# Kernel optimization log

Measured on AMD Instinct MI355X. Metric: run time of the kernel, lower is better.

## Reference

```python
import jax, jax.numpy as jnp
import numpy as np

B, S, E, G, O, TOPK = 4, 2048, 1024, 8, 4096, 2


def setup_inputs() -> dict:
    key = jax.random.key(0)
    k1, k2, k3, k4 = jax.random.split(key, 4)
    return {
        "hidden_states": jax.random.normal(k1, (B, S, E), dtype=jnp.float32),
        "WG": jax.random.normal(k2, (E, G), dtype=jnp.float32) * (1.0 / np.sqrt(E)),
        "Wi": jax.random.normal(k3, (G, E, O), dtype=jnp.float32) * (1.0 / np.sqrt(E)),
        "down": jax.random.normal(k4, (O, E), dtype=jnp.float32) * (1.0 / np.sqrt(O)),
        "topk": TOPK,
    }


def reference(hidden_states, WG, Wi, down, topk):
    # gate logits: [b, s, g]
    gate = jnp.matmul(hidden_states, WG)
    # sparse path (smoe_fwd): topk mask zeroes non-selected gate LOGITS,
    # so non-selected experts get sigmoid(0) = 0.5 (faithful to source).
    _, idx = jax.lax.top_k(gate, topk)              # [b, s, topk]
    mask = jnp.max(jax.nn.one_hot(idx, gate.shape[-1], dtype=gate.dtype), axis=-2)  # [b, s, g]
    w = jax.nn.sigmoid(gate * mask)                  # [b, s, g]
    # weighted combination over all expert matrices: [b, s, o]
    y = jnp.einsum('bse,bsg,geo->bso', hidden_states, w, Wi)
    # squared ReLU
    h = jnp.square(jax.nn.relu(y))
    return jnp.matmul(h, down)                       # [b, s, e]
```

## Files before the change

### kernel.cpp

```cpp
#include <hip/hip_runtime.h>
#include <hip/hip_bf16.h>
#include <math.h>

typedef __bf16 bf16;
typedef __bf16 bf16x4 __attribute__((ext_vector_type(4)));
typedef __bf16 bf16x8 __attribute__((ext_vector_type(8)));
typedef float  floatx4 __attribute__((ext_vector_type(4)));

#define N_TOK 8192
#define E_DIM 1024
#define G_DIM 8
#define O_DIM 4096
#define EPI_LD 132

__device__ __forceinline__ void gload_lds16(const void* g, void* l) {
    __builtin_amdgcn_global_load_lds(
        (__attribute__((address_space(1))) void*)(g),
        (__attribute__((address_space(3))) void*)(l),
        16, 0, 0);
}

__global__ __launch_bounds__(256) void gate_compute(
    const float* __restrict__ X,
    const float* __restrict__ WG,
    int* __restrict__ sel,
    float* __restrict__ sval)
{
    __shared__ float lwgT[G_DIM * E_DIM];
    const int tid  = threadIdx.x;
    const int wave = tid >> 6;
    const int lane = tid & 63;

#pragma unroll
    for (int k = 0; k < 8; ++k) {
        const int i = k * 256 + tid;
        const float4 v = *(const float4*)(WG + i * 4);
        const int e  = i >> 1;
        const int g0 = (i & 1) * 4;
        lwgT[(g0 + 0) * E_DIM + e] = v.x;
        lwgT[(g0 + 1) * E_DIM + e] = v.y;
        lwgT[(g0 + 2) * E_DIM + e] = v.z;
        lwgT[(g0 + 3) * E_DIM + e] = v.w;
    }
    __syncthreads();

    const int t = blockIdx.x * 4 + wave;
    float acc[G_DIM];
#pragma unroll
    for (int g = 0; g < G_DIM; ++g) acc[g] = 0.f;

#pragma unroll
    for (int it = 0; it < 4; ++it) {
        const int e0 = it * 256 + lane * 4;
        const float4 xv = *(const float4*)(X + (long)t * E_DIM + e0);
#pragma unroll
        for (int g = 0; g < G_DIM; ++g) {
            const float4 wv = *(const float4*)(lwgT + g * E_DIM + e0);
            acc[g] += xv.x * wv.x + xv.y * wv.y + xv.z * wv.z + xv.w * wv.w;
        }
    }
#pragma unroll
    for (int g = 0; g < G_DIM; ++g) {
        float v = acc[g];
#pragma unroll
        for (int off = 32; off > 0; off >>= 1) v += __shfl_down(v, off, 64);
        acc[g] = v;
    }
    if (lane == 0) {
        int i1 = 0;
#pragma unroll
        for (int g = 1; g < G_DIM; ++g) if (acc[g] > acc[i1]) i1 = g;
        int i2 = (i1 == 0) ? 1 : 0;
#pragma unroll
        for (int g = 0; g < G_DIM; ++g)
            if (g != i1 && g != i2 && acc[g] > acc[i2]) i2 = g;
#pragma unroll
        for (int s = 0; s < 2; ++s) {
            const int g = s ? i2 : i1;
            sel[t * 2 + s]  = g;
            sval[t * 2 + s] = 1.f / (1.f + expf(-acc[g])) - 0.5f;
        }
    }
}

__global__ __launch_bounds__(1024) void route_kernel(
    const int* __restrict__ sel, const float* __restrict__ sval,
    int* __restrict__ cnt, int* __restrict__ off, int* __restrict__ offp,
    int* __restrict__ tok, float* __restrict__ scl, int* __restrict__ pos)
{
    __shared__ int hcnt[16][G_DIM];
    __shared__ int wbase[16][G_DIM];
    const int tid  = threadIdx.x;
    const int w    = tid >> 6;
    const int lane = tid & 63;
    const unsigned long long below = ((unsigned long long)1 << lane) - 1;

    int c0[G_DIM];
#pragma unroll
    for (int g = 0; g < G_DIM; ++g) c0[g] = 0;
    for (int c = 0; c < 16; ++c) {
        const int g = sel[w * 1024 + c * 64 + lane];
#pragma unroll
        for (int gg = 0; gg < G_DIM; ++gg)
            c0[gg] += __popcll(__ballot(g == gg));
    }
    if (lane == 0)
#pragma unroll
        for (int g = 0; g < G_DIM; ++g) hcnt[w][g] = c0[g];
    __syncthreads();

    if (tid == 0) {
        int tot[G_DIM];
#pragma unroll
        for (int g = 0; g < G_DIM; ++g) {
            int a = 0;
            for (int ww = 0; ww < 16; ++ww) { wbase[ww][g] = a; a += hcnt[ww][g]; }
            tot[g] = a; cnt[g] = a;
        }
        int a = 0, b = 0;
#pragma unroll
        for (int g = 0; g < G_DIM; ++g) {
            off[g]  = a; a += tot[g];
            offp[g] = b; b += (tot[g] + 127) & ~127;
        }
        offp[G_DIM] = b;
    }
    __syncthreads();

    int run[G_DIM];
#pragma unroll
    for (int g = 0; g < G_DIM; ++g) run[g] = 0;
    for (int c = 0; c < 16; ++c) {
        const int idx = w * 1024 + c * 64 + lane;
        const int g   = sel[idx];
        const float sv = sval[idx];
        int myrank = 0;
#pragma unroll
        for (int gg = 0; gg < G_DIM; ++gg) {
            const unsigned long long m = __ballot(g == gg);
            const int r = run[gg] + __popcll(m & below);
            if (g == gg) myrank = r;
            run[gg] += __popcll(m);
        }
        const int p = wbase[w][g] + myrank;
        tok[g * N_TOK + p] = idx >> 1;
        scl[g * N_TOK + p] = sv;
        pos[idx] = (g << 16) | p;
    }
}

__global__ __launch_bounds__(256) void convert_x(
    const float* __restrict__ X, bf16* __restrict__ Xb)
{
    const long i = ((long)blockIdx.x * 256 + threadIdx.x) * 4;
    const float4 v = *(const float4*)(X + i);
    bf16x4 o;
    o[0] = (bf16)v.x; o[1] = (bf16)v.y; o[2] = (bf16)v.z; o[3] = (bf16)v.w;
    *(bf16x4*)(Xb + i) = o;
}

__global__ __launch_bounds__(256) void transpose_conv(
    const float* __restrict__ S, bf16* __restrict__ D, int R, int C)
{
    __shared__ float tile[64][65];
    const int r0  = blockIdx.x * 64;
    const int c0  = blockIdx.y * 64;
    const int tid = threadIdx.x;
    const int tr  = tid >> 4;
    const int tc4 = (tid & 15) * 4;

#pragma unroll
    for (int p = 0; p < 4; ++p) {
        const int r = p * 16 + tr;
        const float4 v = *(const float4*)(S + (long)(r0 + r) * C + c0 + tc4);
        tile[r][tc4 + 0] = v.x;
        tile[r][tc4 + 1] = v.y;
        tile[r][tc4 + 2] = v.z;
        tile[r][tc4 + 3] = v.w;
    }
    __syncthreads();
#pragma unroll
    for (int p = 0; p < 4; ++p) {
        const int c = p * 16 + tr;
        bf16x4 o;
        o[0] = (bf16)tile[tc4 + 0][c];
        o[1] = (bf16)tile[tc4 + 1][c];
        o[2] = (bf16)tile[tc4 + 2][c];
        o[3] = (bf16)tile[tc4 + 3][c];
        *(bf16x4*)(D + (long)(c0 + c) * R + r0 + tc4) = o;
    }
}

__global__ __launch_bounds__(256) void wsum_kernel(
    const bf16* __restrict__ WiT, bf16* __restrict__ WsumT)
{
    const int o  = blockIdx.x;
    const int e4 = threadIdx.x * 4;
    float a0 = 0.f, a1 = 0.f, a2 = 0.f, a3 = 0.f;
#pragma unroll
    for (int g = 0; g < G_DIM; ++g) {
        const bf16x4 v = *(const bf16x4*)(WiT + (long)o * 8192 + g * E_DIM + e4);
        a0 += (float)v[0]; a1 += (float)v[1]; a2 += (float)v[2]; a3 += (float)v[3];
    }
    bf16x4 w;
    w[0] = (bf16)(0.5f * a0); w[1] = (bf16)(0.5f * a1);
    w[2] = (bf16)(0.5f * a2); w[3] = (bf16)(0.5f * a3);
    *(bf16x4*)(WsumT + (long)o * E_DIM + e4) = w;
}

__global__ __launch_bounds__(128) void gather_rows(
    const bf16* __restrict__ Xb, const int* __restrict__ cnt,
    const int* __restrict__ offp, const int* __restrict__ tok,
    bf16* __restrict__ Xs)
{
    const int slot = blockIdx.x;
    if (slot >= offp[G_DIM]) return;
    int g = 0;
    while (slot >= offp[g + 1]) ++g;
    const int p = slot - offp[g];
    bf16* dst = Xs + (long)slot * E_DIM + threadIdx.x * 8;
    if (p < cnt[g]) {
        const bf16* src = Xb + (long)tok[g * N_TOK + p] * E_DIM + threadIdx.x * 8;
        *(bf16x8*)dst = *(const bf16x8*)src;
    } else {
        bf16x8 z = {};
        *(bf16x8*)dst = z;
    }
}

__device__ __forceinline__ void gemm_core256(
    const bf16* __restrict__ Ap, long lda,
    const bf16* __restrict__ Bp, long ldb,
    int K, char* smem, floatx4 (&acc)[8][4])
{
    const int tid  = threadIdx.x;
    const int wave = tid >> 6;
    const int lane = tid & 63;
    const int wm   = wave >> 2;
    const int wn   = wave & 3;
    const int fr   = lane & 15;
    const int fq   = lane >> 4;

#pragma unroll
    for (int i = 0; i < 8; ++i)
#pragma unroll
        for (int j = 0; j < 4; ++j)
            acc[i][j] = (floatx4){0.f, 0.f, 0.f, 0.f};

    const int  srow = tid >> 2;
    const int  ksw  = (((tid & 3) ^ ((tid >> 3) & 3)) << 4);
    const char* sa  = (const char*)Ap + (long)srow * (lda * 2) + ksw;
    const char* sb  = (const char*)Bp + (long)srow * (ldb * 2) + ksw;
    const long aR   = lda * 256;
    const long bR   = ldb * 256;
    const int  ldsW = wave * 1024;

#define STAGE_H(sbase, src, rstr, kb) do {                                   \
        gload_lds16((src) + (kb),          smem + (sbase) + ldsW);           \
        gload_lds16((src) + (kb) + (rstr), smem + (sbase) + 8192 + ldsW);    \
    } while (0)

    const int asw = ((fq ^ ((fr >> 1) & 3)) << 4);
    const int aro = (wm * 128 + fr) * 64 + asw;
    const int bro = (wn * 64 + fr) * 64 + asw;

    const int nt = K >> 6;

    {
        const long k1 = (nt > 1) ? 128 : 0;
        STAGE_H(0,             sa, aR, 0);
        STAGE_H(32768,         sb, bR, 0);
        STAGE_H(16384,         sa, aR, 64);
        STAGE_H(49152,         sb, bR, 64);
        STAGE_H(65536 + 32768, sb, bR, k1);
        STAGE_H(65536 + 0,     sa, aR, k1);
    }
    asm volatile("s_waitcnt vmcnt(4)" ::: "memory");
    __builtin_amdgcn_s_barrier();

#define LD8(v, off) (v) = *(const bf16x8*)(smem + (off))
#define PHASE_MID()   __builtin_amdgcn_s_barrier()
#define PHASE_END()   __builtin_amdgcn_s_barrier()
#define PHASE_END_V() do {                                                   \
        asm volatile("s_waitcnt vmcnt(8)" ::: "memory");                     \
        __builtin_amdgcn_s_barrier();                                        \
    } while (0)

    bf16x8 af[4], bq[4];

    for (int t = 0; t < nt; ++t) {
        const int  bo  = (t & 1) << 16;
        const int  nbo = bo ^ 65536;
        const long k1  = (long)((t + 1 < nt) ? t + 1 : nt - 1) * 128;
        const long k2  = (long)((t + 2 < nt) ? t + 2 : nt - 1) * 128;

#pragma unroll
        for (int i = 0; i < 4; ++i) LD8(af[i], bo + aro + i * 1024);
#pragma unroll
        for (int j = 0; j < 4; ++j) LD8(bq[j], bo + 32768 + bro + j * 1024);
        STAGE_H(nbo + 49152, sb, bR, k1 + 64);
        PHASE_MID();
        __builtin_amdgcn_s_setprio(1);
#pragma unroll
        for (int i = 0; i < 4; ++i)
#pragma unroll
            for (int j = 0; j < 4; ++j)
                acc[i][j] = __builtin_amdgcn_mfma_f32_16x16x32_bf16(
                    af[i], bq[j], acc[i][j], 0, 0, 0);
        __builtin_amdgcn_s_setprio(0);
        PHASE_END();

#pragma unroll
        for (int i = 0; i < 4; ++i) LD8(af[i], bo + aro + 4096 + i * 1024);
        STAGE_H(nbo + 16384, sa, aR, k1 + 64);
        PHASE_MID();
        __builtin_amdgcn_s_setprio(1);
#pragma unroll
        for (int i = 0; i < 4; ++i)
#pragma unroll
            for (int j = 0; j < 4; ++j)
                acc[4 + i][j] = __builtin_amdgcn_mfma_f32_16x16x32_bf16(
                    af[i], bq[j], acc[4 + i][j], 0, 0, 0);
        __builtin_amdgcn_s_setprio(0);
        PHASE_END_V();

#pragma unroll
        for (int i = 0; i < 4; ++i) LD8(af[i], bo + 16384 + aro + i * 1024);
#pragma unroll
        for (int j = 0; j < 4; ++j) LD8(bq[j], bo + 49152 + bro + j * 1024);
        STAGE_H(bo + 32768, sb, bR, k2);
        PHASE_MID();
        __builtin_amdgcn_s_setprio(1);
#pragma unroll
        for (int i = 0; i < 4; ++i)
#pragma unroll
            for (int j = 0; j < 4; ++j)
                acc[i][j] = __builtin_amdgcn_mfma_f32_16x16x32_bf16(
                    af[i], bq[j], acc[i][j], 0, 0, 0);
        __builtin_amdgcn_s_setprio(0);
        PHASE_END();

#pragma unroll
        for (int i = 0; i < 4; ++i) LD8(af[i], bo + 16384 + aro + 4096 + i * 1024);
        STAGE_H(bo + 0, sa, aR, k2);
        PHASE_MID();
        __builtin_amdgcn_s_setprio(1);
#pragma unroll
        for (int i = 0; i < 4; ++i)
#pragma unroll
            for (int j = 0; j < 4; ++j)
                acc[4 + i][j] = __builtin_amdgcn_mfma_f32_16x16x32_bf16(
                    af[i], bq[j], acc[4 + i][j], 0, 0, 0);
        __builtin_amdgcn_s_setprio(0);
        PHASE_END_V();
    }

    asm volatile("s_waitcnt vmcnt(0)" ::: "memory");
    __builtin_amdgcn_s_barrier();
#undef STAGE_H
#undef LD8
#undef PHASE_MID
#undef PHASE_END
#undef PHASE_END_V
}

__global__ __launch_bounds__(512, 2) void gemm256_base(
    const bf16* __restrict__ A, const bf16* __restrict__ BT,
    bf16* __restrict__ C)
{
    __shared__ __align__(16) char smem[131072];
    const int u   = blockIdx.x;
    const int xcd = u & 7;
    const int s   = u >> 3;
    const int mt  = s & 31;
    const int ct  = xcd + 8 * (s >> 5);
    const int row0 = mt * 256, col0 = ct * 256;

    floatx4 acc[8][4];
    gemm_core256(A + (long)row0 * E_DIM, E_DIM,
                 BT + (long)col0 * E_DIM, E_DIM,
                 E_DIM, smem, acc);

    const int tid = threadIdx.x, wave = tid >> 6, lane = tid & 63;
    const int wm = wave >> 2, wn = wave & 3, fr = lane & 15, fq = lane >> 4;
    bf16* tile = (bf16*)smem;
#pragma unroll
    for (int i = 0; i < 8; ++i)
#pragma unroll
        for (int j = 0; j < 4; ++j)
#pragma unroll
            for (int r = 0; r < 4; ++r)
                tile[(wm * 128 + i * 16 + fq * 4 + r) * 256 + wn * 64 + j * 16 + fr] =
                    (bf16)(acc[i][j][r]);
    __syncthreads();
#pragma unroll
    for (int k = 0; k < 16; ++k) {
        const int rl = (tid >> 5) + k * 16;
        const int cc = (tid & 31) * 8;
        *(bf16x8*)(C + (long)(row0 + rl) * O_DIM + col0 + cc) =
            *(const bf16x8*)(tile + rl * 256 + cc);
    }
}

__global__ __launch_bounds__(512, 2) void gemm256_sparse(
    const bf16* __restrict__ Xs,
    const bf16* __restrict__ WiT,
    const int* __restrict__ cnt,
    const int* __restrict__ off,
    const int* __restrict__ offp,
    const float* __restrict__ scl,
    bf16* __restrict__ ysp)
{
    const int u   = blockIdx.x;
    const int xcd = u & 7;
    const int s   = u >> 3;
    const int mt  = s & 63;
    const int pc  = xcd + 8 * (s >> 6);
    const int g   = pc & 7;
    const int ct  = pc >> 3;

    const int cg     = cnt[g];
    const int base_p = offp[g];
    const int cgp    = offp[g + 1] - base_p;
    const int m0     = mt * 256;
    if (m0 >= cgp) return;

    __shared__ __align__(16) char smem[131072];
    const int col0 = ct * 256;

    floatx4 acc[8][4];
    gemm_core256(Xs + (long)(base_p + m0) * E_DIM, E_DIM,
                 WiT + (long)col0 * 8192 + g * E_DIM, 8192,
                 E_DIM, smem, acc);

    const int tid = threadIdx.x, wave = tid >> 6, lane = tid & 63;
    const int wm = wave >> 2, wn = wave & 3, fr = lane & 15, fq = lane >> 4;
    const float* sclg = scl + g * N_TOK;
    const int clmax = cg - 1;
    bf16* tile = (bf16*)smem;
#pragma unroll
    for (int i = 0; i < 8; ++i)
#pragma unroll
        for (int r = 0; r < 4; ++r) {
            const int rl = wm * 128 + i * 16 + fq * 4 + r;
            const int gm = m0 + rl;
            const float sv = sclg[gm > clmax ? clmax : gm];
#pragma unroll
            for (int j = 0; j < 4; ++j)
                tile[rl * 256 + wn * 64 + j * 16 + fr] = (bf16)(sv * acc[i][j][r]);
        }
    __syncthreads();
    const long ob = off[g] + m0;
#pragma unroll
    for (int k = 0; k < 16; ++k) {
        const int rl = (tid >> 5) + k * 16;
        if (m0 + rl < cg) {
            const int cc = (tid & 31) * 8;
            *(bf16x8*)(ysp + (ob + rl) * O_DIM + col0 + cc) =
                *(const bf16x8*)(tile + rl * 256 + cc);
        }
    }
}

template <typename OUT, bool VEC>
__global__ __launch_bounds__(256, 4) void gemm_mt(
    const bf16* __restrict__ A, int lda,
    const bf16* __restrict__ BT, int ldb,
    OUT* __restrict__ C, int ldc, int K)
{
    __shared__ char smem[VEC ? (128 * EPI_LD * 2) : 16384];
    bf16* As = (bf16*)smem;
    bf16* Bs = (bf16*)(smem + 8192);

    const int u   = blockIdx.x;
    const int xcd = u & 7;
    const int s   = u >> 3;
    const int mt  = s & 63;
    const int col = xcd + 8 * (s >> 6);

    const int tid  = threadIdx.x;
    const int wave = tid >> 6;
    const int lane = tid & 63;
    const int row0 = mt * 128;
    const int col0 = col * 128;

    const int sr = lane >> 2;
    const int sc = (lane & 3) * 8;
    const bf16* agp0 = A  + (long)(row0 + 16 * wave       + sr) * lda + sc;
    const bf16* agp1 = A  + (long)(row0 + 16 * (wave + 4) + sr) * lda + sc;
    const bf16* bgp0 = BT + (long)(col0 + 16 * wave       + sr) * ldb + sc;
    const bf16* bgp1 = BT + (long)(col0 + 16 * (wave + 4) + sr) * ldb + sc;
    bf16* asl0 = As + (long)wave * 512;
    bf16* asl1 = As + (long)(wave + 4) * 512;
    bf16* bsl0 = Bs + (long)wave * 512;
    bf16* bsl1 = Bs + (long)(wave + 4) * 512;

    const int mi_base = (wave >> 1) * 64;
    const int ni_base = (wave & 1) * 64;
    const int fr = lane & 15;
    const int fq = lane >> 4;

    floatx4 acc[4][4] = {};

    for (int k0 = 0; k0 < K; k0 += 32) {
        __syncthreads();
        gload_lds16(agp0 + k0, (void*)asl0);
        gload_lds16(agp1 + k0, (void*)asl1);
        gload_lds16(bgp0 + k0, (void*)bsl0);
        gload_lds16(bgp1 + k0, (void*)bsl1);
        __syncthreads();

        bf16x8 af[4], bfr[4];
#pragma unroll
        for (int i = 0; i < 4; ++i) {
            af[i]  = *(const bf16x8*)(As + (mi_base + i * 16 + fr) * 32 + fq * 8);
            bfr[i] = *(const bf16x8*)(Bs + (ni_base + i * 16 + fr) * 32 + fq * 8);
        }
#pragma unroll
        for (int i = 0; i < 4; ++i)
#pragma unroll
            for (int j = 0; j < 4; ++j)
                acc[i][j] = __builtin_amdgcn_mfma_f32_16x16x32_bf16(
                    af[i], bfr[j], acc[i][j], 0, 0, 0);
    }

    if (VEC) {
        __syncthreads();
        bf16* tile = (bf16*)smem;
#pragma unroll
        for (int i = 0; i < 4; ++i)
#pragma unroll
            for (int j = 0; j < 4; ++j)
#pragma unroll
                for (int r = 0; r < 4; ++r) {
                    const int rl = mi_base + i * 16 + fq * 4 + r;
                    const int cl = ni_base + j * 16 + fr;
                    tile[rl * EPI_LD + cl] = (bf16)acc[i][j][r];
                }
        __syncthreads();
#pragma unroll
        for (int k = 0; k < 8; ++k) {
            const int rl = (tid >> 3) + 32 * (k >> 1);
            const int cl = (tid & 7) * 8 + 64 * (k & 1);
            const bf16x8 v = *(const bf16x8*)(tile + rl * EPI_LD + cl);
            *(bf16x8*)((bf16*)C + (long)(row0 + rl) * ldc + col0 + cl) = v;
        }
    } else {
#pragma unroll
        for (int i = 0; i < 4; ++i)
#pragma unroll
            for (int j = 0; j < 4; ++j)
#pragma unroll
                for (int r = 0; r < 4; ++r) {
                    const long row = row0 + mi_base + i * 16 + fq * 4 + r;
                    const long cg  = col0 + ni_base + j * 16 + fr;
                    C[row * ldc + cg] = (OUT)acc[i][j][r];
                }
    }
}

__global__ __launch_bounds__(256) void relu2_gather(
    const bf16* __restrict__ Yb,
    const bf16* __restrict__ ysp,
    const int* __restrict__ pos,
    const int* __restrict__ off,
    bf16* __restrict__ H)
{
    const int t  = blockIdx.x;
    const int p0 = pos[t * 2];
    const int p1 = pos[t * 2 + 1];
    const long r0 = off[p0 >> 16] + (p0 & 0xffff);
    const long r1 = off[p1 >> 16] + (p1 & 0xffff);
    const int c = threadIdx.x * 16;

    const bf16* yb = Yb + (long)t * O_DIM + c;
    const bf16* s0 = ysp + r0 * O_DIM + c;
    const bf16* s1 = ysp + r1 * O_DIM + c;
    bf16* hp = H + (long)t * O_DIM + c;

#pragma unroll
    for (int h = 0; h < 2; ++h) {
        const bf16x8 a = *(const bf16x8*)(yb + h * 8);
        const bf16x8 b = *(const bf16x8*)(s0 + h * 8);
        const bf16x8 d = *(const bf16x8*)(s1 + h * 8);
        bf16x8 o;
#pragma unroll
        for (int k = 0; k < 8; ++k) {
            float v = (float)a[k] + (float)b[k] + (float)d[k];
            v = fmaxf(v, 0.f);
            o[k] = (bf16)(v * v);
        }
        *(bf16x8*)(hp + h * 8) = o;
    }
}

extern "C" void kernel_launch(void* const* d_in, const int* in_sizes, int n_in,
                              void* d_out, int out_size, void* d_ws, size_t ws_size,
                              hipStream_t stream)
{
    const float* X  = (const float*)d_in[0];
    const float* WG = (const float*)d_in[1];
    const float* Wi = (const float*)d_in[2];
    const float* dn = (const float*)d_in[3];
    float* out = (float*)d_out;

    char* ws = (char*)d_ws;
    const long MB = 1l << 20;
    int*   cnt   = (int*)ws;
    int*   off   = (int*)(ws + 1024);
    int*   offp  = (int*)(ws + 2048);
    int*   pos   = (int*)(ws + 4096);
    int*   tok   = (int*)(ws + 128 * 1024);
    float* scl   = (float*)(ws + 448 * 1024);
    int*   sel   = (int*)(ws + 704 * 1024);
    float* sval  = (float*)(ws + 768 * 1024);
    bf16*  dnT   = (bf16*)(ws + 1 * MB);
    bf16*  WiT   = (bf16*)(ws + 9 * MB);
    bf16*  Hh    = (bf16*)(ws + 9 * MB);
    bf16*  Xs    = (bf16*)(ws + 73 * MB);
    bf16*  Yb    = (bf16*)(ws + 107 * MB);
    bf16*  ysp   = (bf16*)(ws + 171 * MB);
    bf16*  Xb    = (bf16*)(ws + 171 * MB);
    bf16*  WsumT = (bf16*)(ws + 187 * MB);

    gate_compute<<<dim3(N_TOK / 4), dim3(256), 0, stream>>>(X, WG, sel, sval);
    route_kernel<<<dim3(1), dim3(1024), 0, stream>>>(sel, sval, cnt, off, offp,
                                                     tok, scl, pos);
    convert_x<<<dim3(N_TOK * E_DIM / 1024), dim3(256), 0, stream>>>(X, Xb);
    transpose_conv<<<dim3(8192 / 64, O_DIM / 64), dim3(256), 0, stream>>>(Wi, WiT, 8192, O_DIM);
    transpose_conv<<<dim3(O_DIM / 64, E_DIM / 64), dim3(256), 0, stream>>>(dn, dnT, O_DIM, E_DIM);
    wsum_kernel<<<dim3(O_DIM), dim3(256), 0, stream>>>(WiT, WsumT);
    gemm256_base<<<dim3(512), dim3(512), 0, stream>>>(Xb, WsumT, Yb);
    gather_rows<<<dim3(17408), dim3(128), 0, stream>>>(Xb, cnt, offp, tok, Xs);
    gemm256_sparse<<<dim3(8192), dim3(512), 0, stream>>>(
        Xs, WiT, cnt, off, offp, scl, ysp);
    relu2_gather<<<dim3(N_TOK), dim3(256), 0, stream>>>(Yb, ysp, pos, off, Hh);
    gemm_mt<float, false><<<dim3(64 * 8), dim3(256), 0, stream>>>(
        Hh, O_DIM, dnT, O_DIM, out, E_DIM, O_DIM);
}
```

Baseline: 718.0 us.

## Restructure GEMM mainloop to whole-tile double buffering with two barriers per iteration

Replaces the interleaved half-tile staging, which used eight barriers per 128-wide K step, with a simpler double-buffered scheme. Each iteration computes on one full buffer, then issues all eight global-to-LDS loads for tile t+2 into the same buffer and synchronises with two barriers. The goal is to cut barrier and sync overhead and let MFMA chains run uninterrupted. The cost is less overlap, since loads for the next-next tile are only issued after compute on the current buffer finishes.

```diff
diff --git a/kernel.cpp b/kernel.cpp
--- a/kernel.cpp
+++ b/kernel.cpp
@@ -255,9 +255,17 @@
     const long bR   = ldb * 256;
     const int  ldsW = wave * 1024;
 
-#define STAGE_H(sbase, src, rstr, kb) do {                                   \
-        gload_lds16((src) + (kb),          smem + (sbase) + ldsW);           \
-        gload_lds16((src) + (kb) + (rstr), smem + (sbase) + 8192 + ldsW);    \
+#define STAGE_T(buf, kt) do {                                                \
+        const long _ko = (long)(kt) * 128;                                   \
+        char* _lb = smem + ((buf) << 16) + ldsW;                             \
+        gload_lds16(sa + _ko,           _lb);                                \
+        gload_lds16(sa + _ko + aR,      _lb + 8192);                         \
+        gload_lds16(sa + _ko + 64,      _lb + 16384);                        \
+        gload_lds16(sa + _ko + aR + 64, _lb + 16384 + 8192);                 \
+        gload_lds16(sb + _ko,           _lb + 32768);                        \
+        gload_lds16(sb + _ko + bR,      _lb + 32768 + 8192);                 \
+        gload_lds16(sb + _ko + 64,      _lb + 49152);                        \
+        gload_lds16(sb + _ko + bR + 64, _lb + 49152 + 8192);                 \
     } while (0)
 
     const int asw = ((fq ^ ((fr >> 1) & 3)) << 4);
@@ -266,40 +274,24 @@
 
     const int nt = K >> 6;
 
-    {
-        const long k1 = (nt > 1) ? 128 : 0;
-        STAGE_H(0,             sa, aR, 0);
-        STAGE_H(32768,         sb, bR, 0);
-        STAGE_H(16384,         sa, aR, 64);
-        STAGE_H(49152,         sb, bR, 64);
-        STAGE_H(65536 + 32768, sb, bR, k1);
-        STAGE_H(65536 + 0,     sa, aR, k1);
-    }
-    asm volatile("s_waitcnt vmcnt(4)" ::: "memory");
+    STAGE_T(0, 0);
+    STAGE_T(1, (nt > 1) ? 1 : 0);
+    asm volatile("s_waitcnt vmcnt(8)" ::: "memory");
+    __builtin_amdgcn_sched_barrier(0);
     __builtin_amdgcn_s_barrier();
+    __builtin_amdgcn_sched_barrier(0);
 
 #define LD8(v, off) (v) = *(const bf16x8*)(smem + (off))
-#define PHASE_MID()   __builtin_amdgcn_s_barrier()
-#define PHASE_END()   __builtin_amdgcn_s_barrier()
-#define PHASE_END_V() do {                                                   \
-        asm volatile("s_waitcnt vmcnt(8)" ::: "memory");                     \
-        __builtin_amdgcn_s_barrier();                                        \
-    } while (0)
 
     bf16x8 af[4], bq[4];
 
     for (int t = 0; t < nt; ++t) {
-        const int  bo  = (t & 1) << 16;
-        const int  nbo = bo ^ 65536;
-        const long k1  = (long)((t + 1 < nt) ? t + 1 : nt - 1) * 128;
-        const long k2  = (long)((t + 2 < nt) ? t + 2 : nt - 1) * 128;
-
+        const int bo = (t & 1) << 16;
+
+#pragma unroll
+        for (int j = 0; j < 4; ++j) LD8(bq[j], bo + 32768 + bro + j * 1024);
 #pragma unroll
         for (int i = 0; i < 4; ++i) LD8(af[i], bo + aro + i * 1024);
-#pragma unroll
-        for (int j = 0; j < 4; ++j) LD8(bq[j], bo + 32768 + bro + j * 1024);
-        STAGE_H(nbo + 49152, sb, bR, k1 + 64);
-        PHASE_MID();
         __builtin_amdgcn_s_setprio(1);
 #pragma unroll
         for (int i = 0; i < 4; ++i)
@@ -308,12 +300,8 @@
                 acc[i][j] = __builtin_amdgcn_mfma_f32_16x16x32_bf16(
                     af[i], bq[j], acc[i][j], 0, 0, 0);
         __builtin_amdgcn_s_setprio(0);
-        PHASE_END();
-
 #pragma unroll
         for (int i = 0; i < 4; ++i) LD8(af[i], bo + aro + 4096 + i * 1024);
-        STAGE_H(nbo + 16384, sa, aR, k1 + 64);
-        PHASE_MID();
         __builtin_amdgcn_s_setprio(1);
 #pragma unroll
         for (int i = 0; i < 4; ++i)
@@ -322,14 +310,13 @@
                 acc[4 + i][j] = __builtin_amdgcn_mfma_f32_16x16x32_bf16(
                     af[i], bq[j], acc[4 + i][j], 0, 0, 0);
         __builtin_amdgcn_s_setprio(0);
-        PHASE_END_V();
-
+
+        __builtin_amdgcn_sched_barrier(0);
+
+#pragma unroll
+        for (int j = 0; j < 4; ++j) LD8(bq[j], bo + 49152 + bro + j * 1024);
 #pragma unroll
         for (int i = 0; i < 4; ++i) LD8(af[i], bo + 16384 + aro + i * 1024);
-#pragma unroll
-        for (int j = 0; j < 4; ++j) LD8(bq[j], bo + 49152 + bro + j * 1024);
-        STAGE_H(bo + 32768, sb, bR, k2);
-        PHASE_MID();
         __builtin_amdgcn_s_setprio(1);
 #pragma unroll
         for (int i = 0; i < 4; ++i)
@@ -338,12 +325,8 @@
                 acc[i][j] = __builtin_amdgcn_mfma_f32_16x16x32_bf16(
                     af[i], bq[j], acc[i][j], 0, 0, 0);
         __builtin_amdgcn_s_setprio(0);
-        PHASE_END();
-
 #pragma unroll
         for (int i = 0; i < 4; ++i) LD8(af[i], bo + 16384 + aro + 4096 + i * 1024);
-        STAGE_H(bo + 0, sa, aR, k2);
-        PHASE_MID();
         __builtin_amdgcn_s_setprio(1);
 #pragma unroll
         for (int i = 0; i < 4; ++i)
@@ -352,16 +335,25 @@
                 acc[4 + i][j] = __builtin_amdgcn_mfma_f32_16x16x32_bf16(
                     af[i], bq[j], acc[4 + i][j], 0, 0, 0);
         __builtin_amdgcn_s_setprio(0);
-        PHASE_END_V();
+
+        __builtin_amdgcn_sched_barrier(0);
+        __builtin_amdgcn_s_barrier();
+        __builtin_amdgcn_sched_barrier(0);
+        if (t + 2 < nt) {
+            STAGE_T(t & 1, t + 2);
+            asm volatile("s_waitcnt vmcnt(8)" ::: "memory");
+        } else if (t + 1 < nt) {
+            asm volatile("s_waitcnt vmcnt(0)" ::: "memory");
+        }
+        __builtin_amdgcn_sched_barrier(0);
+        __builtin_amdgcn_s_barrier();
+        __builtin_amdgcn_sched_barrier(0);
     }
 
     asm volatile("s_waitcnt vmcnt(0)" ::: "memory");
     __builtin_amdgcn_s_barrier();
-#undef STAGE_H
+#undef STAGE_T
 #undef LD8
-#undef PHASE_MID
-#undef PHASE_END
-#undef PHASE_END_V
 }
 
 __global__ __launch_bounds__(512, 2) void gemm256_base(
```

Measured after the change: 738.2 us. +2.8%, slower.

## Fuse X conversion into gate and Wi transpose with expert-weight sum

Applied to the files above, without the earlier changes.

The gate kernel now also writes the bf16 copy of X, which removes a separate conversion pass that re-read X. Wi transpose and the summed-expert weight are computed in one kernel, so the bf16 WiT is no longer read back to build WsumT. The sum is now accumulated from fp32 values instead of bf16. Gather and relu2 kernels handle several rows per 512-thread block to cut block count.

```diff
diff --git a/kernel.cpp b/kernel.cpp
--- a/kernel.cpp
+++ b/kernel.cpp
@@ -24,7 +24,8 @@
     const float* __restrict__ X,
     const float* __restrict__ WG,
     int* __restrict__ sel,
-    float* __restrict__ sval)
+    float* __restrict__ sval,
+    bf16* __restrict__ Xb)
 {
     __shared__ float lwgT[G_DIM * E_DIM];
     const int tid  = threadIdx.x;
@@ -53,6 +54,10 @@
     for (int it = 0; it < 4; ++it) {
         const int e0 = it * 256 + lane * 4;
         const float4 xv = *(const float4*)(X + (long)t * E_DIM + e0);
+        bf16x4 xo;
+        xo[0] = (bf16)xv.x; xo[1] = (bf16)xv.y;
+        xo[2] = (bf16)xv.z; xo[3] = (bf16)xv.w;
+        *(bf16x4*)(Xb + (long)t * E_DIM + e0) = xo;
 #pragma unroll
         for (int g = 0; g < G_DIM; ++g) {
             const float4 wv = *(const float4*)(lwgT + g * E_DIM + e0);
@@ -147,16 +152,6 @@
         scl[g * N_TOK + p] = sv;
         pos[idx] = (g << 16) | p;
     }
-}
-
-__global__ __launch_bounds__(256) void convert_x(
-    const float* __restrict__ X, bf16* __restrict__ Xb)
-{
-    const long i = ((long)blockIdx.x * 256 + threadIdx.x) * 4;
-    const float4 v = *(const float4*)(X + i);
-    bf16x4 o;
-    o[0] = (bf16)v.x; o[1] = (bf16)v.y; o[2] = (bf16)v.z; o[3] = (bf16)v.w;
-    *(bf16x4*)(Xb + i) = o;
 }
 
 __global__ __launch_bounds__(256) void transpose_conv(
@@ -191,36 +186,70 @@
     }
 }
 
-__global__ __launch_bounds__(256) void wsum_kernel(
-    const bf16* __restrict__ WiT, bf16* __restrict__ WsumT)
-{
-    const int o  = blockIdx.x;
-    const int e4 = threadIdx.x * 4;
-    float a0 = 0.f, a1 = 0.f, a2 = 0.f, a3 = 0.f;
-#pragma unroll
+__global__ __launch_bounds__(256) void transpose_wi_wsum(
+    const float* __restrict__ Wi,
+    bf16* __restrict__ WiT,
+    bf16* __restrict__ WsumT)
+{
+    __shared__ float tile[64][65];
+    const int e0  = blockIdx.x * 64;
+    const int c0  = blockIdx.y * 64;
+    const int tid = threadIdx.x;
+    const int tr  = tid >> 4;
+    const int tc4 = (tid & 15) * 4;
+
+    float acc[4][4] = {};
+
     for (int g = 0; g < G_DIM; ++g) {
-        const bf16x4 v = *(const bf16x4*)(WiT + (long)o * 8192 + g * E_DIM + e4);
-        a0 += (float)v[0]; a1 += (float)v[1]; a2 += (float)v[2]; a3 += (float)v[3];
-    }
-    bf16x4 w;
-    w[0] = (bf16)(0.5f * a0); w[1] = (bf16)(0.5f * a1);
-    w[2] = (bf16)(0.5f * a2); w[3] = (bf16)(0.5f * a3);
-    *(bf16x4*)(WsumT + (long)o * E_DIM + e4) = w;
-}
-
-__global__ __launch_bounds__(128) void gather_rows(
+        __syncthreads();
+#pragma unroll
+        for (int p = 0; p < 4; ++p) {
+            const int r = p * 16 + tr;
+            const float4 v = *(const float4*)(
+                Wi + (long)(g * 1024 + e0 + r) * O_DIM + c0 + tc4);
+            tile[r][tc4 + 0] = v.x;
+            tile[r][tc4 + 1] = v.y;
+            tile[r][tc4 + 2] = v.z;
+            tile[r][tc4 + 3] = v.w;
+        }
+        __syncthreads();
+#pragma unroll
+        for (int p = 0; p < 4; ++p) {
+            const int c = p * 16 + tr;
+            bf16x4 o;
+#pragma unroll
+            for (int k = 0; k < 4; ++k) {
+                const float f = tile[tc4 + k][c];
+                o[k] = (bf16)f;
+                acc[p][k] += f;
+            }
+            *(bf16x4*)(WiT + (long)(c0 + c) * 8192 + g * 1024 + e0 + tc4) = o;
+        }
+    }
+#pragma unroll
+    for (int p = 0; p < 4; ++p) {
+        const int c = p * 16 + tr;
+        bf16x4 w;
+#pragma unroll
+        for (int k = 0; k < 4; ++k) w[k] = (bf16)(0.5f * acc[p][k]);
+        *(bf16x4*)(WsumT + (long)(c0 + c) * E_DIM + e0 + tc4) = w;
+    }
+}
+
+__global__ __launch_bounds__(512) void gather_rows(
     const bf16* __restrict__ Xb, const int* __restrict__ cnt,
     const int* __restrict__ offp, const int* __restrict__ tok,
     bf16* __restrict__ Xs)
 {
-    const int slot = blockIdx.x;
+    const int slot = blockIdx.x * 4 + (threadIdx.x >> 7);
+    const int l    = threadIdx.x & 127;
     if (slot >= offp[G_DIM]) return;
     int g = 0;
     while (slot >= offp[g + 1]) ++g;
     const int p = slot - offp[g];
-    bf16* dst = Xs + (long)slot * E_DIM + threadIdx.x * 8;
+    bf16* dst = Xs + (long)slot * E_DIM + l * 8;
     if (p < cnt[g]) {
-        const bf16* src = Xb + (long)tok[g * N_TOK + p] * E_DIM + threadIdx.x * 8;
+        const bf16* src = Xb + (long)tok[g * N_TOK + p] * E_DIM + l * 8;
         *(bf16x8*)dst = *(const bf16x8*)src;
     } else {
         bf16x8 z = {};
@@ -559,19 +588,19 @@
     }
 }
 
-__global__ __launch_bounds__(256) void relu2_gather(
+__global__ __launch_bounds__(512) void relu2_gather(
     const bf16* __restrict__ Yb,
     const bf16* __restrict__ ysp,
     const int* __restrict__ pos,
     const int* __restrict__ off,
     bf16* __restrict__ H)
 {
-    const int t  = blockIdx.x;
+    const int t  = blockIdx.x * 2 + (threadIdx.x >> 8);
     const int p0 = pos[t * 2];
     const int p1 = pos[t * 2 + 1];
     const long r0 = off[p0 >> 16] + (p0 & 0xffff);
     const long r1 = off[p1 >> 16] + (p1 & 0xffff);
-    const int c = threadIdx.x * 16;
+    const int c = (threadIdx.x & 255) * 16;
 
     const bf16* yb = Yb + (long)t * O_DIM + c;
     const bf16* s0 = ysp + r0 * O_DIM + c;
@@ -623,18 +652,17 @@
     bf16*  Xb    = (bf16*)(ws + 171 * MB);
     bf16*  WsumT = (bf16*)(ws + 187 * MB);
 
-    gate_compute<<<dim3(N_TOK / 4), dim3(256), 0, stream>>>(X, WG, sel, sval);
+    gate_compute<<<dim3(N_TOK / 4), dim3(256), 0, stream>>>(X, WG, sel, sval, Xb);
     route_kernel<<<dim3(1), dim3(1024), 0, stream>>>(sel, sval, cnt, off, offp,
                                                      tok, scl, pos);
-    convert_x<<<dim3(N_TOK * E_DIM / 1024), dim3(256), 0, stream>>>(X, Xb);
-    transpose_conv<<<dim3(8192 / 64, O_DIM / 64), dim3(256), 0, stream>>>(Wi, WiT, 8192, O_DIM);
+    transpose_wi_wsum<<<dim3(E_DIM / 64, O_DIM / 64), dim3(256), 0, stream>>>(
+        Wi, WiT, WsumT);
     transpose_conv<<<dim3(O_DIM / 64, E_DIM / 64), dim3(256), 0, stream>>>(dn, dnT, O_DIM, E_DIM);
-    wsum_kernel<<<dim3(O_DIM), dim3(256), 0, stream>>>(WiT, WsumT);
     gemm256_base<<<dim3(512), dim3(512), 0, stream>>>(Xb, WsumT, Yb);
-    gather_rows<<<dim3(17408), dim3(128), 0, stream>>>(Xb, cnt, offp, tok, Xs);
+    gather_rows<<<dim3(17408 / 4), dim3(512), 0, stream>>>(Xb, cnt, offp, tok, Xs);
     gemm256_sparse<<<dim3(8192), dim3(512), 0, stream>>>(
         Xs, WiT, cnt, off, offp, scl, ysp);
-    relu2_gather<<<dim3(N_TOK), dim3(256), 0, stream>>>(Yb, ysp, pos, off, Hh);
+    relu2_gather<<<dim3(N_TOK / 2), dim3(512), 0, stream>>>(Yb, ysp, pos, off, Hh);
     gemm_mt<float, false><<<dim3(64 * 8), dim3(256), 0, stream>>>(
         Hh, O_DIM, dnT, O_DIM, out, E_DIM, O_DIM);
 }
```

Result: no change. 722.9 us (+0.7%).
